# Performance work log

Hardware: AMD Instinct MI355X
Metric: run time of the kernel (lower is better)

Reference implementation:

```python
import jax, jax.numpy as jnp
import numpy as np

B = 512        # batch of parallel sequences
TM1 = 64       # T-1 recurrence steps
BELIEF = 2048  # GRU / deterministic belief size
STATE = 256    # stochastic state size
ACTION = 64
HIDDEN = 2048
EMB = 1024     # embedding_size['fusion']
MIN_STD = 0.1


def setup_inputs() -> dict:
    key = jax.random.key(0)
    ks = jax.random.split(key, 16)
    w = lambda k, shape: jax.random.normal(k, shape, dtype=jnp.float32) * 0.02
    return {
        "prev_state": jax.random.normal(ks[0], (B, STATE), dtype=jnp.float32),
        "actions": jax.random.normal(ks[1], (TM1, B, ACTION), dtype=jnp.float32),
        "prev_belief": jax.random.normal(ks[2], (B, BELIEF), dtype=jnp.float32),
        "obs_emb": jax.random.normal(ks[3], (TM1, B, EMB), dtype=jnp.float32),
        "nonterminals": jnp.ones((TM1, B, 1), dtype=jnp.float32),
        # fc_embed_state_action
        "W_embed": w(ks[4], (STATE + ACTION, BELIEF)),
        "b_embed": jnp.zeros((BELIEF,), jnp.float32),
        # GRUCell (input-to-hidden / hidden-to-hidden, gate order r,z,n as torch)
        "Wi": w(ks[5], (BELIEF, 3 * BELIEF)),
        "bi": jnp.zeros((3 * BELIEF,), jnp.float32),
        "Wh": w(ks[6], (BELIEF, 3 * BELIEF)),
        "bh": jnp.zeros((3 * BELIEF,), jnp.float32),
        # stochastic_state_model (prior): h -> hidden -> 2*state
        "W1": w(ks[7], (BELIEF, HIDDEN)),
        "b1": jnp.zeros((HIDDEN,), jnp.float32),
        "W2": w(ks[8], (HIDDEN, 2 * STATE)),
        "b2": jnp.zeros((2 * STATE,), jnp.float32),
        # obs_encoder (posterior): cat(h, obs_emb) -> hidden -> 2*state
        "W1p": w(ks[9], (BELIEF + EMB, HIDDEN)),
        "b1p": jnp.zeros((HIDDEN,), jnp.float32),
        "W2p": w(ks[10], (HIDDEN, 2 * STATE)),
        "b2p": jnp.zeros((2 * STATE,), jnp.float32),
        # reparameterized-sampling noise (rsample = loc + scale * eps)
        "eps_prior": jax.random.normal(ks[11], (TM1, B, STATE), dtype=jnp.float32),
        "eps_post": jax.random.normal(ks[12], (TM1, B, STATE), dtype=jnp.float32),
    }


def reference(prev_state, actions, prev_belief, obs_emb, nonterminals,
              W_embed, b_embed, Wi, bi, Wh, bh,
              W1, b1, W2, b2, W1p, b1p, W2p, b2p,
              eps_prior, eps_post):
    def step(carry, xs):
        belief, post_state = carry
        a, obs, nt, ep, eq = xs
        s = post_state * nt                                   # [B, S]
        hidden = jax.nn.relu(jnp.concatenate([s, a], axis=1) @ W_embed + b_embed)
        # torch.nn.GRUCell math (gate order r, z, n)
        gi = hidden @ Wi + bi
        gh = belief @ Wh + bh
        i_r, i_z, i_n = jnp.split(gi, 3, axis=1)
        h_r, h_z, h_n = jnp.split(gh, 3, axis=1)
        r = jax.nn.sigmoid(i_r + h_r)
        z = jax.nn.sigmoid(i_z + h_z)
        n = jnp.tanh(i_n + r * h_n)
        new_belief = (1.0 - z) * n + z * belief               # [B, H]
        # prior stochastic state model
        hp = jax.nn.relu(new_belief @ W1 + b1)
        loc_p, raw_p = jnp.split(hp @ W2 + b2, 2, axis=1)
        scale_p = jax.nn.softplus(raw_p) + MIN_STD
        prior_state = loc_p + scale_p * ep                    # rsample
        # posterior from obs embedding
        hq = jax.nn.relu(jnp.concatenate([new_belief, obs], axis=1) @ W1p + b1p)
        loc_q, raw_q = jnp.split(hq @ W2p + b2p, 2, axis=1)
        scale_q = jax.nn.softplus(raw_q) + MIN_STD
        post_new = loc_q + scale_q * eq                       # rsample
        ys = (new_belief, prior_state, loc_p, scale_p, post_new, loc_q, scale_q)
        return (new_belief, post_new), ys

    _, ys = jax.lax.scan(step, (prev_belief, prev_state),
                         (actions, obs_emb, nonterminals, eps_prior, eps_post))
    # (beliefs, prior_states, prior_means, prior_std_devs,
    #  posterior_states, posterior_means, posterior_std_devs), each [T-1, B, ...]
    return ys
```

## Files before the change

kernel.cpp:

```cpp
#include <hip/hip_runtime.h>
#include <hip/hip_bf16.h>
#include <cstdint>

typedef __hip_bfloat16 bf16;
typedef __attribute__((ext_vector_type(8))) short bf16x8v;
typedef __attribute__((ext_vector_type(4))) float f32x4;

#define TM1 64
#define BATCH 512
#define BELIEF 2048
#define STATE 256
#define ACTION 64
#define HIDDEN 2048
#define EMB 1024

#define OUT_BEL  ((size_t)0)
#define OUT_PST  ((size_t)67108864)
#define OUT_PMU  ((size_t)75497472)
#define OUT_PSD  ((size_t)83886080)
#define OUT_QST  ((size_t)92274688)
#define OUT_QMU  ((size_t)100663296)
#define OUT_QSD  ((size_t)109051904)

__device__ __forceinline__ void gload_lds16(const bf16* g, bf16* l) {
  __builtin_amdgcn_global_load_lds(
      (const __attribute__((address_space(1))) unsigned int*)g,
      (__attribute__((address_space(3))) unsigned int*)l, 16, 0, 0);
}

__device__ __forceinline__ unsigned short bfb(float f) {
  bf16 h = __float2bfloat16(f);
  return *reinterpret_cast<unsigned short*>(&h);
}

struct GDesc {
  const bf16* A; const bf16* B; const float* bias; void* C;
  int M, N, K, mode, nb;
};

template<int BM, int BN>
__global__ __launch_bounds__(256)
void gemm2(GDesc d0, GDesc d1)
{
  const int nwg = gridDim.x;
  const int orig = blockIdx.x;
  const int q8 = nwg >> 3, r8 = nwg & 7;
  const int xcd = orig & 7, oo = orig >> 3;
  int bid = (xcd < r8 ? xcd * (q8 + 1) : r8 * (q8 + 1) + (xcd - r8) * q8) + oo;

  GDesc d = d0;
  if (bid >= d.nb) { bid -= d.nb; d = d1; }

  const int nm = d.M / BM;
  const int mb = bid % nm;
  const int nbk = bid / nm;
  const int m0 = mb * BM, n0 = nbk * BN;

  __shared__ __align__(16) bf16 sA[2][BM * 64];
  __shared__ __align__(16) bf16 sB[2][BN * 64];

  const int tid = threadIdx.x;
  const int lane = tid & 63;
  const int wid = tid >> 6;
  const int wm = wid >> 1, wn = wid & 1;
  const int lr = lane & 15;
  const int ko = (lane >> 4) * 8;
  constexpr int WMt = BM / 2, WNt = BN / 2;
  constexpr int MR = WMt / 16, NR = WNt / 16;

  const bf16* Abase = d.A + (size_t)m0 * d.K;
  const bf16* Bbase = d.B + (size_t)n0 * d.K;
  const int K = d.K;

  auto stage = [&](int buf, int k0) {
    #pragma unroll
    for (int i = 0; i < BM / 32; ++i) {
      int c = i * 256 + tid;
      gload_lds16(Abase + (size_t)(c >> 3) * K + k0 + (c & 7) * 8, &sA[buf][c * 8]);
    }
    #pragma unroll
    for (int i = 0; i < BN / 32; ++i) {
      int c = i * 256 + tid;
      gload_lds16(Bbase + (size_t)(c >> 3) * K + k0 + (c & 7) * 8, &sB[buf][c * 8]);
    }
  };

  f32x4 acc[MR][NR] = {};

  stage(0, 0);
  __syncthreads();
  const int nk = K >> 6;
  for (int it = 0; it < nk; ++it) {
    const int cur = it & 1;
    if (it + 1 < nk) stage(cur ^ 1, (it + 1) << 6);
    #pragma unroll
    for (int kk = 0; kk < 2; ++kk) {
      bf16x8v af[MR], bfv[NR];
      #pragma unroll
      for (int m = 0; m < MR; ++m)
        af[m] = *(const bf16x8v*)&sA[cur][(wm * WMt + m * 16 + lr) * 64 + kk * 32 + ko];
      #pragma unroll
      for (int n = 0; n < NR; ++n)
        bfv[n] = *(const bf16x8v*)&sB[cur][(wn * WNt + n * 16 + lr) * 64 + kk * 32 + ko];
      #pragma unroll
      for (int m = 0; m < MR; ++m)
        #pragma unroll
        for (int n = 0; n < NR; ++n)
          acc[m][n] = __builtin_amdgcn_mfma_f32_16x16x32_bf16(af[m], bfv[n], acc[m][n], 0, 0, 0);
    }
    __syncthreads();
  }

  const int r0 = (lane >> 4) * 4;
  #pragma unroll
  for (int m = 0; m < MR; ++m) {
    #pragma unroll
    for (int n = 0; n < NR; ++n) {
      int gc = n0 + wn * WNt + n * 16 + lr;
      float bv = d.bias[gc];
      #pragma unroll
      for (int r = 0; r < 4; ++r) {
        int gr = m0 + wm * WMt + m * 16 + r0 + r;
        float v = acc[m][n][r] + bv;
        if (d.mode == 1)
          ((bf16*)d.C)[(size_t)gr * d.N + gc] = __float2bfloat16(v > 0.f ? v : 0.f);
        else
          ((float*)d.C)[(size_t)gr * d.N + gc] = v;
      }
    }
  }
}

__global__ __launch_bounds__(256)
void w2p_post(const bf16* __restrict__ hq, const bf16* __restrict__ W2pT,
              const float* __restrict__ b2p, const float* __restrict__ eps,
              float* __restrict__ o_mu, float* __restrict__ o_sd,
              float* __restrict__ o_st,
              const float* __restrict__ nt_next, const float* __restrict__ act_next,
              bf16* __restrict__ xcat, int make_xcat)
{
  constexpr int K = 2048, NK = K / 64;
  const int mb = blockIdx.x & 7, nl = blockIdx.x >> 3;
  const int m0 = mb * 64;

  __shared__ __align__(16) char smem[49152];
  bf16 (*sA)[64 * 64]  = (bf16(*)[64 * 64])smem;
  bf16 (*sB)[128 * 64] = (bf16(*)[128 * 64])(smem + 16384);
  float* tile = (float*)smem;

  const int tid = threadIdx.x;
  const int lane = tid & 63;
  const int wid = tid >> 6;
  const int wm = wid >> 1, wn = wid & 1;
  const int lr = lane & 15;
  const int ko = (lane >> 4) * 8;

  const bf16* Abase = hq + (size_t)m0 * K;

  auto stage = [&](int buf, int k0) {
    #pragma unroll
    for (int i = 0; i < 2; ++i) {
      int c = i * 256 + tid;
      gload_lds16(Abase + (size_t)(c >> 3) * K + k0 + (c & 7) * 8, &sA[buf][c * 8]);
    }
    #pragma unroll
    for (int i = 0; i < 4; ++i) {
      int c = i * 256 + tid;
      int row = c >> 3;
      int grow = (row < 64) ? (nl * 64 + row) : (192 + nl * 64 + row);
      gload_lds16(W2pT + (size_t)grow * K + k0 + (c & 7) * 8, &sB[buf][c * 8]);
    }
  };

  f32x4 acc[2][4] = {};
  stage(0, 0);
  __syncthreads();
  for (int it = 0; it < NK; ++it) {
    const int cur = it & 1;
    if (it + 1 < NK) stage(cur ^ 1, (it + 1) << 6);
    #pragma unroll
    for (int kk = 0; kk < 2; ++kk) {
      bf16x8v af[2], bfv[4];
      #pragma unroll
      for (int m = 0; m < 2; ++m)
        af[m] = *(const bf16x8v*)&sA[cur][(wm * 32 + m * 16 + lr) * 64 + kk * 32 + ko];
      #pragma unroll
      for (int n = 0; n < 4; ++n)
        bfv[n] = *(const bf16x8v*)&sB[cur][(wn * 64 + n * 16 + lr) * 64 + kk * 32 + ko];
      #pragma unroll
      for (int m = 0; m < 2; ++m)
        #pragma unroll
        for (int n = 0; n < 4; ++n)
          acc[m][n] = __builtin_amdgcn_mfma_f32_16x16x32_bf16(af[m], bfv[n], acc[m][n], 0, 0, 0);
    }
    __syncthreads();
  }

  const int r0 = (lane >> 4) * 4;
  #pragma unroll
  for (int m = 0; m < 2; ++m)
    #pragma unroll
    for (int n = 0; n < 4; ++n) {
      int tc = wn * 64 + n * 16 + lr;
      #pragma unroll
      for (int r = 0; r < 4; ++r)
        tile[(wm * 32 + m * 16 + r0 + r) * 128 + tc] = acc[m][n][r];
    }
  __syncthreads();

  for (int e = tid; e < 4096; e += 256) {
    int rr = e >> 6, cc = e & 63;
    int b = m0 + rr;
    int j = nl * 64 + cc;
    float loc = tile[rr * 128 + cc] + b2p[j];
    float raw = tile[rr * 128 + 64 + cc] + b2p[256 + j];
    float sp = (raw > 20.f) ? raw : log1pf(__expf(raw));
    float scale = sp + 0.1f;
    float st = loc + scale * eps[(size_t)b * 256 + j];
    o_mu[(size_t)b * 256 + j] = loc;
    o_sd[(size_t)b * 256 + j] = scale;
    o_st[(size_t)b * 256 + j] = st;
    if (make_xcat) {
      xcat[(size_t)b * 320 + j] = __float2bfloat16(st * nt_next[b]);
      if (nl == 0)
        xcat[(size_t)b * 320 + 256 + cc] = __float2bfloat16(act_next[(size_t)b * 64 + cc]);
    }
  }
}

__global__ void transpose_cvt(const float* __restrict__ src, bf16* __restrict__ dst,
                              int K, int N)
{
  __shared__ float t[32][33];
  int n0 = blockIdx.x * 32, k0 = blockIdx.y * 32;
  int tx = threadIdx.x, ty = threadIdx.y;
  #pragma unroll
  for (int i = 0; i < 32; i += 8)
    t[ty + i][tx] = src[(size_t)(k0 + ty + i) * N + n0 + tx];
  __syncthreads();
  #pragma unroll
  for (int i = 0; i < 32; i += 8)
    dst[(size_t)(n0 + ty + i) * K + k0 + tx] = __float2bfloat16(t[tx][ty + i]);
}

__global__ void init_belief(const float* __restrict__ prev_belief,
                            float* __restrict__ bf32, bf16* __restrict__ bb16)
{
  int i = blockIdx.x * 256 + threadIdx.x;
  float v = prev_belief[i];
  bf32[i] = v;
  bb16[i] = __float2bfloat16(v);
}

__global__ void xcat0_kernel(const float* __restrict__ prev_state,
                             const float* __restrict__ nt0,
                             const float* __restrict__ act0,
                             bf16* __restrict__ xcat)
{
  int idx = blockIdx.x * 256 + threadIdx.x;
  if (idx >= BATCH * 320) return;
  int b = idx / 320;
  int c = idx - b * 320;
  float v;
  if (c < STATE) v = prev_state[b * STATE + c] * nt0[b];
  else           v = act0[b * ACTION + (c - STATE)];
  xcat[idx] = __float2bfloat16(v);
}

__device__ __forceinline__ float sigmoidf_(float x) { return 1.f / (1.f + __expf(-x)); }

__device__ __forceinline__ float gru1(float ir, float hr, float iz, float hz,
                                      float in_, float hn, float bo)
{
  float r = sigmoidf_(ir + hr);
  float z = sigmoidf_(iz + hz);
  float n = tanhf(in_ + r * hn);
  return (1.f - z) * n + z * bo;
}

__global__ void gru_ew(const float* __restrict__ gi, const float* __restrict__ gh,
                       float* __restrict__ belief, float* __restrict__ out_bel,
                       bf16* __restrict__ belief_b16, bf16* __restrict__ hqcat,
                       const float* __restrict__ obs_t)
{
  int i = blockIdx.x * 256 + threadIdx.x;
  int b = i >> 9;
  int c = (i & 511) * 4;
  size_t gb = (size_t)b * 6144;
  float4 ir = *(const float4*)&gi[gb + c];
  float4 iz = *(const float4*)&gi[gb + 2048 + c];
  float4 in_ = *(const float4*)&gi[gb + 4096 + c];
  float4 hr = *(const float4*)&gh[gb + c];
  float4 hz = *(const float4*)&gh[gb + 2048 + c];
  float4 hn = *(const float4*)&gh[gb + 4096 + c];
  float4 bo = *(const float4*)&belief[(size_t)b * 2048 + c];
  float4 nb;
  nb.x = gru1(ir.x, hr.x, iz.x, hz.x, in_.x, hn.x, bo.x);
  nb.y = gru1(ir.y, hr.y, iz.y, hz.y, in_.y, hn.y, bo.y);
  nb.z = gru1(ir.z, hr.z, iz.z, hz.z, in_.z, hn.z, bo.z);
  nb.w = gru1(ir.w, hr.w, iz.w, hz.w, in_.w, hn.w, bo.w);
  *(float4*)&belief[(size_t)b * 2048 + c] = nb;
  *(float4*)&out_bel[(size_t)b * 2048 + c] = nb;
  ushort4 u; u.x = bfb(nb.x); u.y = bfb(nb.y); u.z = bfb(nb.z); u.w = bfb(nb.w);
  *(ushort4*)&belief_b16[(size_t)b * 2048 + c] = u;
  *(ushort4*)&hqcat[(size_t)b * 3072 + c] = u;
  if ((i & 511) < 256) {
    float4 ov = *(const float4*)&obs_t[(size_t)b * 1024 + c];
    ushort4 uo; uo.x = bfb(ov.x); uo.y = bfb(ov.y); uo.z = bfb(ov.z); uo.w = bfb(ov.w);
    *(ushort4*)&hqcat[(size_t)b * 3072 + 2048 + c] = uo;
  }
}

__global__ void cvt_f32_bf16(const float* __restrict__ src, bf16* __restrict__ dst)
{
  int i = blockIdx.x * 256 + threadIdx.x;
  float4 v = *(const float4*)&src[i * 4];
  ushort4 u; u.x = bfb(v.x); u.y = bfb(v.y); u.z = bfb(v.z); u.w = bfb(v.w);
  *(ushort4*)&dst[i * 4] = u;
}

__global__ void prior_ew(const float* __restrict__ yp, const float* __restrict__ eps,
                         float* __restrict__ o_mu, float* __restrict__ o_sd,
                         float* __restrict__ o_st)
{
  int idx = blockIdx.x * 256 + threadIdx.x;
  int r = idx >> 8;
  int j = idx & 255;
  float loc = yp[(size_t)r * 512 + j];
  float raw = yp[(size_t)r * 512 + 256 + j];
  float sp = (raw > 20.f) ? raw : log1pf(__expf(raw));
  float scale = sp + 0.1f;
  o_mu[idx] = loc;
  o_sd[idx] = scale;
  o_st[idx] = loc + scale * eps[idx];
}

extern "C" void kernel_launch(void* const* d_in, const int* in_sizes, int n_in,
                              void* d_out, int out_size, void* d_ws, size_t ws_size,
                              hipStream_t stream)
{
  (void)in_sizes; (void)n_in; (void)out_size; (void)ws_size;
  const float* prev_state = (const float*)d_in[0];
  const float* actions    = (const float*)d_in[1];
  const float* prev_belief= (const float*)d_in[2];
  const float* obs_emb    = (const float*)d_in[3];
  const float* nonterm    = (const float*)d_in[4];
  const float* W_embed    = (const float*)d_in[5];
  const float* b_embed    = (const float*)d_in[6];
  const float* Wi         = (const float*)d_in[7];
  const float* bi         = (const float*)d_in[8];
  const float* Wh         = (const float*)d_in[9];
  const float* bh         = (const float*)d_in[10];
  const float* W1         = (const float*)d_in[11];
  const float* b1         = (const float*)d_in[12];
  const float* W2         = (const float*)d_in[13];
  const float* b2         = (const float*)d_in[14];
  const float* W1p        = (const float*)d_in[15];
  const float* b1p        = (const float*)d_in[16];
  const float* W2p        = (const float*)d_in[17];
  const float* b2p        = (const float*)d_in[18];
  const float* eps_p      = (const float*)d_in[19];
  const float* eps_q      = (const float*)d_in[20];
  float* out = (float*)d_out;

  char* ws = (char*)d_ws;
  size_t off = 0;
  auto alloc = [&](size_t bytes) -> char* {
    char* p = ws + off;
    off = (off + bytes + 255) & ~(size_t)255;
    return p;
  };
  bf16* WembT = (bf16*)alloc((size_t)2048 * 320 * 2);
  bf16* WiT   = (bf16*)alloc((size_t)6144 * 2048 * 2);
  bf16* WhT   = (bf16*)alloc((size_t)6144 * 2048 * 2);
  bf16* W1T   = (bf16*)alloc((size_t)2048 * 2048 * 2);
  bf16* W2T   = (bf16*)alloc((size_t)512 * 2048 * 2);
  bf16* W1pT  = (bf16*)alloc((size_t)2048 * 3072 * 2);
  bf16* W2pT  = (bf16*)alloc((size_t)512 * 2048 * 2);
  float* belief_f32 = (float*)alloc((size_t)BATCH * BELIEF * 4);
  bf16*  belief_b16 = (bf16*)alloc((size_t)BATCH * BELIEF * 2);
  bf16*  xcat       = (bf16*)alloc((size_t)BATCH * 320 * 2);
  bf16*  hidden     = (bf16*)alloc((size_t)BATCH * BELIEF * 2);
  float* gi         = (float*)alloc((size_t)BATCH * 3 * BELIEF * 4);
  float* gh         = (float*)alloc((size_t)BATCH * 3 * BELIEF * 4);
  bf16*  hqcat      = (bf16*)alloc((size_t)BATCH * 3072 * 2);
  bf16*  hq         = (bf16*)alloc((size_t)BATCH * HIDDEN * 2);
  bf16*  belA       = (bf16*)alloc((size_t)4096 * BELIEF * 2);
  bf16*  hp         = (bf16*)alloc((size_t)4096 * HIDDEN * 2);
  float* yp         = (float*)alloc((size_t)4096 * 512 * 4);

  auto mk = [](const bf16* A, const bf16* B, const float* bias, void* C,
               int M, int N, int K, int mode, int BM, int BN) {
    GDesc g; g.A = A; g.B = B; g.bias = bias; g.C = C;
    g.M = M; g.N = N; g.K = K; g.mode = mode;
    g.nb = (M / BM) * (N / BN);
    return g;
  };
  GDesc dz{}; dz.nb = 0;

  dim3 tb(32, 8);
  transpose_cvt<<<dim3(2048/32, 320/32),  tb, 0, stream>>>(W_embed, WembT, 320, 2048);
  transpose_cvt<<<dim3(6144/32, 2048/32), tb, 0, stream>>>(Wi, WiT, 2048, 6144);
  transpose_cvt<<<dim3(6144/32, 2048/32), tb, 0, stream>>>(Wh, WhT, 2048, 6144);
  transpose_cvt<<<dim3(2048/32, 2048/32), tb, 0, stream>>>(W1, W1T, 2048, 2048);
  transpose_cvt<<<dim3(512/32, 2048/32),  tb, 0, stream>>>(W2, W2T, 2048, 512);
  transpose_cvt<<<dim3(2048/32, 3072/32), tb, 0, stream>>>(W1p, W1pT, 3072, 2048);
  transpose_cvt<<<dim3(512/32, 2048/32),  tb, 0, stream>>>(W2p, W2pT, 2048, 512);

  init_belief<<<(BATCH * BELIEF) / 256, 256, 0, stream>>>(prev_belief, belief_f32, belief_b16);
  xcat0_kernel<<<(BATCH * 320 + 255) / 256, 256, 0, stream>>>(prev_state, nonterm, actions, xcat);

  {
    GDesc e = mk(xcat, WembT, b_embed, hidden, 512, 2048, 320, 1, 64, 64);
    gemm2<64,64><<<e.nb, 256, 0, stream>>>(e, dz);
  }

  for (int t = 0; t < TM1; ++t) {
    GDesc a0 = mk(hidden, WiT, bi, gi, 512, 6144, 2048, 0, 128, 96);
    GDesc a1 = mk(belief_b16, WhT, bh, gh, 512, 6144, 2048, 0, 128, 96);
    gemm2<128,96><<<a0.nb + a1.nb, 256, 0, stream>>>(a0, a1);

    gru_ew<<<1024, 256, 0, stream>>>(
        gi, gh, belief_f32,
        out + OUT_BEL + (size_t)t * BATCH * BELIEF,
        belief_b16, hqcat, obs_emb + (size_t)t * BATCH * EMB);

    GDesc b0 = mk(hqcat, W1pT, b1p, hq, 512, 2048, 3072, 1, 64, 64);
    gemm2<64,64><<<b0.nb, 256, 0, stream>>>(b0, dz);

    int tn = (t < TM1 - 1) ? t + 1 : t;
    w2p_post<<<32, 256, 0, stream>>>(
        hq, W2pT, b2p,
        eps_q + (size_t)t * BATCH * STATE,
        out + OUT_QMU + (size_t)t * BATCH * STATE,
        out + OUT_QSD + (size_t)t * BATCH * STATE,
        out + OUT_QST + (size_t)t * BATCH * STATE,
        nonterm + (size_t)tn * BATCH,
        actions + (size_t)tn * BATCH * ACTION,
        xcat, (t < TM1 - 1) ? 1 : 0);

    if (t < TM1 - 1) {
      GDesc e = mk(xcat, WembT, b_embed, hidden, 512, 2048, 320, 1, 64, 64);
      gemm2<64,64><<<e.nb, 256, 0, stream>>>(e, dz);
    }
  }

  for (int c = 0; c < 8; ++c) {
    const float* belsrc = out + OUT_BEL + (size_t)c * 4096 * BELIEF;
    cvt_f32_bf16<<<(4096 * BELIEF / 4) / 256, 256, 0, stream>>>(belsrc, belA);
    GDesc p1 = mk(belA, W1T, b1, hp, 4096, 2048, 2048, 1, 128, 128);
    gemm2<128,128><<<p1.nb, 256, 0, stream>>>(p1, dz);
    GDesc p2 = mk(hp, W2T, b2, yp, 4096, 512, 2048, 0, 64, 64);
    gemm2<64,64><<<p2.nb, 256, 0, stream>>>(p2, dz);
    prior_ew<<<4096, 256, 0, stream>>>(
        yp, eps_p + (size_t)c * 4096 * STATE,
        out + OUT_PMU + (size_t)c * 4096 * STATE,
        out + OUT_PSD + (size_t)c * 4096 * STATE,
        out + OUT_PST + (size_t)c * 4096 * STATE);
  }
}
```

Before: 10.02 ms.

## Fuse all stages into one persistent kernel with grid-wide atomic barriers

```diff
diff --git a/kernel.cpp b/kernel.cpp
--- a/kernel.cpp
+++ b/kernel.cpp
@@ -6,13 +6,9 @@
 typedef __attribute__((ext_vector_type(8))) short bf16x8v;
 typedef __attribute__((ext_vector_type(4))) float f32x4;
 
+#define NB 256
 #define TM1 64
 #define BATCH 512
-#define BELIEF 2048
-#define STATE 256
-#define ACTION 64
-#define HIDDEN 2048
-#define EMB 1024
 
 #define OUT_BEL  ((size_t)0)
 #define OUT_PST  ((size_t)67108864)
@@ -33,33 +29,29 @@
   return *reinterpret_cast<unsigned short*>(&h);
 }
 
-struct GDesc {
-  const bf16* A; const bf16* B; const float* bias; void* C;
-  int M, N, K, mode, nb;
-};
+__device__ __forceinline__ void gbar(unsigned* cnt, unsigned target) {
+  __syncthreads();
+  if (threadIdx.x == 0) {
+    __threadfence();
+    __hip_atomic_fetch_add(cnt, 1u, __ATOMIC_RELAXED, __HIP_MEMORY_SCOPE_AGENT);
+    while (__hip_atomic_load(cnt, __ATOMIC_RELAXED, __HIP_MEMORY_SCOPE_AGENT) < target)
+      __builtin_amdgcn_s_sleep(2);
+    __threadfence();
+  }
+  __syncthreads();
+}
 
 template<int BM, int BN>
-__global__ __launch_bounds__(256)
-void gemm2(GDesc d0, GDesc d1)
-{
-  const int nwg = gridDim.x;
-  const int orig = blockIdx.x;
-  const int q8 = nwg >> 3, r8 = nwg & 7;
-  const int xcd = orig & 7, oo = orig >> 3;
-  int bid = (xcd < r8 ? xcd * (q8 + 1) : r8 * (q8 + 1) + (xcd - r8) * q8) + oo;
-
-  GDesc d = d0;
-  if (bid >= d.nb) { bid -= d.nb; d = d1; }
-
-  const int nm = d.M / BM;
-  const int mb = bid % nm;
-  const int nbk = bid / nm;
-  const int m0 = mb * BM, n0 = nbk * BN;
-
-  __shared__ __align__(16) bf16 sA[2][BM * 64];
-  __shared__ __align__(16) bf16 sB[2][BN * 64];
-
-  const int tid = threadIdx.x;
+__device__ void gemm_tile(const bf16* __restrict__ A, const bf16* __restrict__ B,
+                          const float* __restrict__ bias, void* __restrict__ C,
+                          int N, int K, int nm, int mode, int job, int tid,
+                          char* pool)
+{
+  bf16 (*sA)[BM * 64] = (bf16(*)[BM * 64])pool;
+  bf16 (*sB)[BN * 64] = (bf16(*)[BN * 64])(pool + 2 * BM * 64 * 2);
+
+  const int m0 = (job % nm) * BM;
+  const int n0 = (job / nm) * BN;
   const int lane = tid & 63;
   const int wid = tid >> 6;
   const int wm = wid >> 1, wn = wid & 1;
@@ -68,9 +60,8 @@
   constexpr int WMt = BM / 2, WNt = BN / 2;
   constexpr int MR = WMt / 16, NR = WNt / 16;
 
-  const bf16* Abase = d.A + (size_t)m0 * d.K;
-  const bf16* Bbase = d.B + (size_t)n0 * d.K;
-  const int K = d.K;
+  const bf16* Abase = A + (size_t)m0 * K;
+  const bf16* Bbase = B + (size_t)n0 * K;
 
   auto stage = [&](int buf, int k0) {
     #pragma unroll
@@ -86,7 +77,7 @@
   };
 
   f32x4 acc[MR][NR] = {};
-
+  __syncthreads();
   stage(0, 0);
   __syncthreads();
   const int nk = K >> 6;
@@ -117,38 +108,37 @@
     #pragma unroll
     for (int n = 0; n < NR; ++n) {
       int gc = n0 + wn * WNt + n * 16 + lr;
-      float bv = d.bias[gc];
+      float bv = bias[gc];
       #pragma unroll
       for (int r = 0; r < 4; ++r) {
         int gr = m0 + wm * WMt + m * 16 + r0 + r;
         float v = acc[m][n][r] + bv;
-        if (d.mode == 1)
-          ((bf16*)d.C)[(size_t)gr * d.N + gc] = __float2bfloat16(v > 0.f ? v : 0.f);
+        if (mode == 1)
+          ((bf16*)C)[(size_t)gr * N + gc] = __float2bfloat16(v > 0.f ? v : 0.f);
         else
-          ((float*)d.C)[(size_t)gr * d.N + gc] = v;
+          ((float*)C)[(size_t)gr * N + gc] = v;
       }
     }
   }
 }
 
-__global__ __launch_bounds__(256)
-void w2p_post(const bf16* __restrict__ hq, const bf16* __restrict__ W2pT,
-              const float* __restrict__ b2p, const float* __restrict__ eps,
-              float* __restrict__ o_mu, float* __restrict__ o_sd,
-              float* __restrict__ o_st,
-              const float* __restrict__ nt_next, const float* __restrict__ act_next,
-              bf16* __restrict__ xcat, int make_xcat)
+__device__ void w2p_tile(const bf16* __restrict__ hq, const bf16* __restrict__ W2pT,
+                         const float* __restrict__ b2p, const float* __restrict__ eps,
+                         float* __restrict__ o_mu, float* __restrict__ o_sd,
+                         float* __restrict__ o_st,
+                         const float* __restrict__ nt_next,
+                         const float* __restrict__ act_next,
+                         bf16* __restrict__ xcat, int make_xcat,
+                         int blk, int tid, char* pool)
 {
   constexpr int K = 2048, NK = K / 64;
-  const int mb = blockIdx.x & 7, nl = blockIdx.x >> 3;
+  const int mb = blk & 7, nl = blk >> 3;
   const int m0 = mb * 64;
 
-  __shared__ __align__(16) char smem[49152];
-  bf16 (*sA)[64 * 64]  = (bf16(*)[64 * 64])smem;
-  bf16 (*sB)[128 * 64] = (bf16(*)[128 * 64])(smem + 16384);
-  float* tile = (float*)smem;
-
-  const int tid = threadIdx.x;
+  bf16 (*sA)[64 * 64]  = (bf16(*)[64 * 64])pool;
+  bf16 (*sB)[128 * 64] = (bf16(*)[128 * 64])(pool + 16384);
+  float* tile = (float*)pool;
+
   const int lane = tid & 63;
   const int wid = tid >> 6;
   const int wm = wid >> 1, wn = wid & 1;
@@ -173,6 +163,7 @@
   };
 
   f32x4 acc[2][4] = {};
+  __syncthreads();
   stage(0, 0);
   __syncthreads();
   for (int it = 0; it < NK; ++it) {
@@ -228,43 +219,23 @@
   }
 }
 
-__global__ void transpose_cvt(const float* __restrict__ src, bf16* __restrict__ dst,
-                              int K, int N)
-{
-  __shared__ float t[32][33];
-  int n0 = blockIdx.x * 32, k0 = blockIdx.y * 32;
-  int tx = threadIdx.x, ty = threadIdx.y;
-  #pragma unroll
-  for (int i = 0; i < 32; i += 8)
-    t[ty + i][tx] = src[(size_t)(k0 + ty + i) * N + n0 + tx];
-  __syncthreads();
-  #pragma unroll
-  for (int i = 0; i < 32; i += 8)
-    dst[(size_t)(n0 + ty + i) * K + k0 + tx] = __float2bfloat16(t[tx][ty + i]);
-}
-
-__global__ void init_belief(const float* __restrict__ prev_belief,
-                            float* __restrict__ bf32, bf16* __restrict__ bb16)
-{
-  int i = blockIdx.x * 256 + threadIdx.x;
-  float v = prev_belief[i];
-  bf32[i] = v;
-  bb16[i] = __float2bfloat16(v);
-}
-
-__global__ void xcat0_kernel(const float* __restrict__ prev_state,
-                             const float* __restrict__ nt0,
-                             const float* __restrict__ act0,
-                             bf16* __restrict__ xcat)
-{
-  int idx = blockIdx.x * 256 + threadIdx.x;
-  if (idx >= BATCH * 320) return;
-  int b = idx / 320;
-  int c = idx - b * 320;
-  float v;
-  if (c < STATE) v = prev_state[b * STATE + c] * nt0[b];
-  else           v = act0[b * ACTION + (c - STATE)];
-  xcat[idx] = __float2bfloat16(v);
+__device__ void transpose_phase(const float* __restrict__ src, bf16* __restrict__ dst,
+                                int K, int N, int bid, int tid, float* t )
+{
+  const int ntile = (K / 32) * (N / 32);
+  const int tx = tid & 31, ty = tid >> 5;
+  for (int it = bid; it < ntile; it += NB) {
+    int kt = it % (K / 32), nt = it / (K / 32);
+    int k0 = kt * 32, n0 = nt * 32;
+    __syncthreads();
+    #pragma unroll
+    for (int i = 0; i < 32; i += 8)
+      t[(ty + i) * 33 + tx] = src[(size_t)(k0 + ty + i) * N + n0 + tx];
+    __syncthreads();
+    #pragma unroll
+    for (int i = 0; i < 32; i += 8)
+      dst[(size_t)(n0 + ty + i) * K + k0 + tx] = __float2bfloat16(t[tx * 33 + ty + i]);
+  }
 }
 
 __device__ __forceinline__ float sigmoidf_(float x) { return 1.f / (1.f + __expf(-x)); }
@@ -278,61 +249,140 @@
   return (1.f - z) * n + z * bo;
 }
 
-__global__ void gru_ew(const float* __restrict__ gi, const float* __restrict__ gh,
-                       float* __restrict__ belief, float* __restrict__ out_bel,
-                       bf16* __restrict__ belief_b16, bf16* __restrict__ hqcat,
-                       const float* __restrict__ obs_t)
-{
-  int i = blockIdx.x * 256 + threadIdx.x;
-  int b = i >> 9;
-  int c = (i & 511) * 4;
-  size_t gb = (size_t)b * 6144;
-  float4 ir = *(const float4*)&gi[gb + c];
-  float4 iz = *(const float4*)&gi[gb + 2048 + c];
-  float4 in_ = *(const float4*)&gi[gb + 4096 + c];
-  float4 hr = *(const float4*)&gh[gb + c];
-  float4 hz = *(const float4*)&gh[gb + 2048 + c];
-  float4 hn = *(const float4*)&gh[gb + 4096 + c];
-  float4 bo = *(const float4*)&belief[(size_t)b * 2048 + c];
-  float4 nb;
-  nb.x = gru1(ir.x, hr.x, iz.x, hz.x, in_.x, hn.x, bo.x);
-  nb.y = gru1(ir.y, hr.y, iz.y, hz.y, in_.y, hn.y, bo.y);
-  nb.z = gru1(ir.z, hr.z, iz.z, hz.z, in_.z, hn.z, bo.z);
-  nb.w = gru1(ir.w, hr.w, iz.w, hz.w, in_.w, hn.w, bo.w);
-  *(float4*)&belief[(size_t)b * 2048 + c] = nb;
-  *(float4*)&out_bel[(size_t)b * 2048 + c] = nb;
-  ushort4 u; u.x = bfb(nb.x); u.y = bfb(nb.y); u.z = bfb(nb.z); u.w = bfb(nb.w);
-  *(ushort4*)&belief_b16[(size_t)b * 2048 + c] = u;
-  *(ushort4*)&hqcat[(size_t)b * 3072 + c] = u;
-  if ((i & 511) < 256) {
-    float4 ov = *(const float4*)&obs_t[(size_t)b * 1024 + c];
-    ushort4 uo; uo.x = bfb(ov.x); uo.y = bfb(ov.y); uo.z = bfb(ov.z); uo.w = bfb(ov.w);
-    *(ushort4*)&hqcat[(size_t)b * 3072 + 2048 + c] = uo;
-  }
-}
-
-__global__ void cvt_f32_bf16(const float* __restrict__ src, bf16* __restrict__ dst)
-{
-  int i = blockIdx.x * 256 + threadIdx.x;
-  float4 v = *(const float4*)&src[i * 4];
-  ushort4 u; u.x = bfb(v.x); u.y = bfb(v.y); u.z = bfb(v.z); u.w = bfb(v.w);
-  *(ushort4*)&dst[i * 4] = u;
-}
-
-__global__ void prior_ew(const float* __restrict__ yp, const float* __restrict__ eps,
-                         float* __restrict__ o_mu, float* __restrict__ o_sd,
-                         float* __restrict__ o_st)
-{
-  int idx = blockIdx.x * 256 + threadIdx.x;
-  int r = idx >> 8;
-  int j = idx & 255;
-  float loc = yp[(size_t)r * 512 + j];
-  float raw = yp[(size_t)r * 512 + 256 + j];
-  float sp = (raw > 20.f) ? raw : log1pf(__expf(raw));
-  float scale = sp + 0.1f;
-  o_mu[idx] = loc;
-  o_sd[idx] = scale;
-  o_st[idx] = loc + scale * eps[idx];
+struct Args {
+  const float *prev_state, *actions, *prev_belief, *obs_emb, *nonterm;
+  const float *W_embed, *b_embed, *Wi, *bi, *Wh, *bh;
+  const float *W1, *b1, *W2, *b2, *W1p, *b1p, *W2p, *b2p;
+  const float *eps_p, *eps_q;
+  bf16 *WembT, *WiT, *WhT, *W1T, *W2T, *W1pT, *W2pT;
+  float* belief_f32; bf16 *belief_b16, *xcat, *hidden;
+  float *gi, *gh; bf16 *hqcat, *hq, *belA, *hp; float* yp;
+  float* out;
+  unsigned* cnt;
+};
+
+__global__ __launch_bounds__(256) void mega(Args a)
+{
+  extern __shared__ char pool[];
+  const int bid = blockIdx.x;
+  const int tid = threadIdx.x;
+  const int sj = ((bid & 7) << 5) | (bid >> 3);
+  unsigned tgt = 0;
+
+  transpose_phase(a.W_embed, a.WembT, 320, 2048, bid, tid, (float*)pool);
+  transpose_phase(a.Wi,  a.WiT,  2048, 6144, bid, tid, (float*)pool);
+  transpose_phase(a.Wh,  a.WhT,  2048, 6144, bid, tid, (float*)pool);
+  transpose_phase(a.W1,  a.W1T,  2048, 2048, bid, tid, (float*)pool);
+  transpose_phase(a.W2,  a.W2T,  2048, 512,  bid, tid, (float*)pool);
+  transpose_phase(a.W1p, a.W1pT, 3072, 2048, bid, tid, (float*)pool);
+  transpose_phase(a.W2p, a.W2pT, 2048, 512,  bid, tid, (float*)pool);
+  for (int i = bid * 256 + tid; i < 512 * 2048; i += NB * 256) {
+    float v = a.prev_belief[i];
+    a.belief_f32[i] = v;
+    a.belief_b16[i] = __float2bfloat16(v);
+  }
+  for (int i = bid * 256 + tid; i < 512 * 320; i += NB * 256) {
+    int b = i / 320, c = i - b * 320;
+    float v = (c < 256) ? a.prev_state[b * 256 + c] * a.nonterm[b]
+                        : a.actions[b * 64 + (c - 256)];
+    a.xcat[i] = __float2bfloat16(v);
+  }
+  gbar(a.cnt, tgt += NB);
+
+  gemm_tile<64, 64>(a.xcat, a.WembT, a.b_embed, a.hidden, 2048, 320, 8, 1, sj, tid, pool);
+  gbar(a.cnt, tgt += NB);
+
+  for (int t = 0; t < TM1; ++t) {
+    gemm_tile<128, 96>(a.hidden, a.WiT, a.bi, a.gi, 6144, 2048, 4, 0, sj, tid, pool);
+    gemm_tile<128, 96>(a.belief_b16, a.WhT, a.bh, a.gh, 6144, 2048, 4, 0, sj, tid, pool);
+    gbar(a.cnt, tgt += NB);
+
+    {
+      const float* obs_t = a.obs_emb + (size_t)t * 512 * 1024;
+      float* out_bel = a.out + OUT_BEL + (size_t)t * 512 * 2048;
+      for (int i = bid * 256 + tid; i < 512 * 2048 / 4; i += NB * 256) {
+        int b = i >> 9;
+        int c = (i & 511) * 4;
+        size_t gb = (size_t)b * 6144;
+        float4 ir = *(const float4*)&a.gi[gb + c];
+        float4 iz = *(const float4*)&a.gi[gb + 2048 + c];
+        float4 in_ = *(const float4*)&a.gi[gb + 4096 + c];
+        float4 hr = *(const float4*)&a.gh[gb + c];
+        float4 hz = *(const float4*)&a.gh[gb + 2048 + c];
+        float4 hn = *(const float4*)&a.gh[gb + 4096 + c];
+        float4 bo = *(const float4*)&a.belief_f32[(size_t)b * 2048 + c];
+        float4 nb;
+        nb.x = gru1(ir.x, hr.x, iz.x, hz.x, in_.x, hn.x, bo.x);
+        nb.y = gru1(ir.y, hr.y, iz.y, hz.y, in_.y, hn.y, bo.y);
+        nb.z = gru1(ir.z, hr.z, iz.z, hz.z, in_.z, hn.z, bo.z);
+        nb.w = gru1(ir.w, hr.w, iz.w, hz.w, in_.w, hn.w, bo.w);
+        *(float4*)&a.belief_f32[(size_t)b * 2048 + c] = nb;
+        *(float4*)&out_bel[(size_t)b * 2048 + c] = nb;
+        ushort4 u; u.x = bfb(nb.x); u.y = bfb(nb.y); u.z = bfb(nb.z); u.w = bfb(nb.w);
+        *(ushort4*)&a.belief_b16[(size_t)b * 2048 + c] = u;
+        *(ushort4*)&a.hqcat[(size_t)b * 3072 + c] = u;
+        if ((i & 511) < 256) {
+          float4 ov = *(const float4*)&obs_t[(size_t)b * 1024 + c];
+          ushort4 uo; uo.x = bfb(ov.x); uo.y = bfb(ov.y); uo.z = bfb(ov.z); uo.w = bfb(ov.w);
+          *(ushort4*)&a.hqcat[(size_t)b * 3072 + 2048 + c] = uo;
+        }
+      }
+    }
+    gbar(a.cnt, tgt += NB);
+
+    gemm_tile<64, 64>(a.hqcat, a.W1pT, a.b1p, a.hq, 2048, 3072, 8, 1, sj, tid, pool);
+    gbar(a.cnt, tgt += NB);
+
+    {
+      int tn = (t < TM1 - 1) ? t + 1 : t;
+      if (bid < 32)
+        w2p_tile(a.hq, a.W2pT, a.b2p,
+                 a.eps_q + (size_t)t * 512 * 256,
+                 a.out + OUT_QMU + (size_t)t * 512 * 256,
+                 a.out + OUT_QSD + (size_t)t * 512 * 256,
+                 a.out + OUT_QST + (size_t)t * 512 * 256,
+                 a.nonterm + (size_t)tn * 512,
+                 a.actions + (size_t)tn * 512 * 64,
+                 a.xcat, (t < TM1 - 1) ? 1 : 0, bid, tid, pool);
+    }
+    gbar(a.cnt, tgt += NB);
+
+    if (t < TM1 - 1) {
+      gemm_tile<64, 64>(a.xcat, a.WembT, a.b_embed, a.hidden, 2048, 320, 8, 1, sj, tid, pool);
+      gbar(a.cnt, tgt += NB);
+    }
+  }
+
+  for (int c = 0; c < 8; ++c) {
+    const float* bsrc = a.out + OUT_BEL + (size_t)c * 4096 * 2048;
+    for (int i = bid * 256 + tid; i < 4096 * 2048 / 4; i += NB * 256) {
+      float4 v = *(const float4*)&bsrc[i * 4];
+      ushort4 u; u.x = bfb(v.x); u.y = bfb(v.y); u.z = bfb(v.z); u.w = bfb(v.w);
+      *(ushort4*)&a.belA[i * 4] = u;
+    }
+    gbar(a.cnt, tgt += NB);
+
+    gemm_tile<128, 128>(a.belA, a.W1T, a.b1, a.hp, 2048, 2048, 32, 1, sj, tid, pool);
+    gemm_tile<128, 128>(a.belA, a.W1T, a.b1, a.hp, 2048, 2048, 32, 1, sj + 256, tid, pool);
+    gbar(a.cnt, tgt += NB);
+
+    gemm_tile<64, 64>(a.hp, a.W2T, a.b2, a.yp, 512, 2048, 64, 0, sj, tid, pool);
+    gemm_tile<64, 64>(a.hp, a.W2T, a.b2, a.yp, 512, 2048, 64, 0, sj + 256, tid, pool);
+    gbar(a.cnt, tgt += NB);
+
+    for (int i = bid * 256 + tid; i < 4096 * 256; i += NB * 256) {
+      int r = i >> 8, j = i & 255;
+      float loc = a.yp[(size_t)r * 512 + j];
+      float raw = a.yp[(size_t)r * 512 + 256 + j];
+      float sp = (raw > 20.f) ? raw : log1pf(__expf(raw));
+      float scale = sp + 0.1f;
+      size_t o = (size_t)c * 4096 * 256 + i;
+      a.out[OUT_PMU + o] = loc;
+      a.out[OUT_PSD + o] = scale;
+      a.out[OUT_PST + o] = loc + scale * a.eps_p[o];
+    }
+    gbar(a.cnt, tgt += NB);
+  }
 }
 
 extern "C" void kernel_launch(void* const* d_in, const int* in_sizes, int n_in,
@@ -340,28 +390,29 @@
                               hipStream_t stream)
 {
   (void)in_sizes; (void)n_in; (void)out_size; (void)ws_size;
-  const float* prev_state = (const float*)d_in[0];
-  const float* actions    = (const float*)d_in[1];
-  const float* prev_belief= (const float*)d_in[2];
-  const float* obs_emb    = (const float*)d_in[3];
-  const float* nonterm    = (const float*)d_in[4];
-  const float* W_embed    = (const float*)d_in[5];
-  const float* b_embed    = (const float*)d_in[6];
-  const float* Wi         = (const float*)d_in[7];
-  const float* bi         = (const float*)d_in[8];
-  const float* Wh         = (const float*)d_in[9];
-  const float* bh         = (const float*)d_in[10];
-  const float* W1         = (const float*)d_in[11];
-  const float* b1         = (const float*)d_in[12];
-  const float* W2         = (const float*)d_in[13];
-  const float* b2         = (const float*)d_in[14];
-  const float* W1p        = (const float*)d_in[15];
-  const float* b1p        = (const float*)d_in[16];
-  const float* W2p        = (const float*)d_in[17];
-  const float* b2p        = (const float*)d_in[18];
-  const float* eps_p      = (const float*)d_in[19];
-  const float* eps_q      = (const float*)d_in[20];
-  float* out = (float*)d_out;
+  Args a;
+  a.prev_state = (const float*)d_in[0];
+  a.actions    = (const float*)d_in[1];
+  a.prev_belief= (const float*)d_in[2];
+  a.obs_emb    = (const float*)d_in[3];
+  a.nonterm    = (const float*)d_in[4];
+  a.W_embed    = (const float*)d_in[5];
+  a.b_embed    = (const float*)d_in[6];
+  a.Wi         = (const float*)d_in[7];
+  a.bi         = (const float*)d_in[8];
+  a.Wh         = (const float*)d_in[9];
+  a.bh         = (const float*)d_in[10];
+  a.W1         = (const float*)d_in[11];
+  a.b1         = (const float*)d_in[12];
+  a.W2         = (const float*)d_in[13];
+  a.b2         = (const float*)d_in[14];
+  a.W1p        = (const float*)d_in[15];
+  a.b1p        = (const float*)d_in[16];
+  a.W2p        = (const float*)d_in[17];
+  a.b2p        = (const float*)d_in[18];
+  a.eps_p      = (const float*)d_in[19];
+  a.eps_q      = (const float*)d_in[20];
+  a.out        = (float*)d_out;
 
   char* ws = (char*)d_ws;
   size_t off = 0;
@@ -370,92 +421,26 @@
     off = (off + bytes + 255) & ~(size_t)255;
     return p;
   };
-  bf16* WembT = (bf16*)alloc((size_t)2048 * 320 * 2);
-  bf16* WiT   = (bf16*)alloc((size_t)6144 * 2048 * 2);
-  bf16* WhT   = (bf16*)alloc((size_t)6144 * 2048 * 2);
-  bf16* W1T   = (bf16*)alloc((size_t)2048 * 2048 * 2);
-  bf16* W2T   = (bf16*)alloc((size_t)512 * 2048 * 2);
-  bf16* W1pT  = (bf16*)alloc((size_t)2048 * 3072 * 2);
-  bf16* W2pT  = (bf16*)alloc((size_t)512 * 2048 * 2);
-  float* belief_f32 = (float*)alloc((size_t)BATCH * BELIEF * 4);
-  bf16*  belief_b16 = (bf16*)alloc((size_t)BATCH * BELIEF * 2);
-  bf16*  xcat       = (bf16*)alloc((size_t)BATCH * 320 * 2);
-  bf16*  hidden     = (bf16*)alloc((size_t)BATCH * BELIEF * 2);
-  float* gi         = (float*)alloc((size_t)BATCH * 3 * BELIEF * 4);
-  float* gh         = (float*)alloc((size_t)BATCH * 3 * BELIEF * 4);
-  bf16*  hqcat      = (bf16*)alloc((size_t)BATCH * 3072 * 2);
-  bf16*  hq         = (bf16*)alloc((size_t)BATCH * HIDDEN * 2);
-  bf16*  belA       = (bf16*)alloc((size_t)4096 * BELIEF * 2);
-  bf16*  hp         = (bf16*)alloc((size_t)4096 * HIDDEN * 2);
-  float* yp         = (float*)alloc((size_t)4096 * 512 * 4);
-
-  auto mk = [](const bf16* A, const bf16* B, const float* bias, void* C,
-               int M, int N, int K, int mode, int BM, int BN) {
-    GDesc g; g.A = A; g.B = B; g.bias = bias; g.C = C;
-    g.M = M; g.N = N; g.K = K; g.mode = mode;
-    g.nb = (M / BM) * (N / BN);
-    return g;
-  };
-  GDesc dz{}; dz.nb = 0;
-
-  dim3 tb(32, 8);
-  transpose_cvt<<<dim3(2048/32, 320/32),  tb, 0, stream>>>(W_embed, WembT, 320, 2048);
-  transpose_cvt<<<dim3(6144/32, 2048/32), tb, 0, stream>>>(Wi, WiT, 2048, 6144);
-  transpose_cvt<<<dim3(6144/32, 2048/32), tb, 0, stream>>>(Wh, WhT, 2048, 6144);
-  transpose_cvt<<<dim3(2048/32, 2048/32), tb, 0, stream>>>(W1, W1T, 2048, 2048);
-  transpose_cvt<<<dim3(512/32, 2048/32),  tb, 0, stream>>>(W2, W2T, 2048, 512);
-  transpose_cvt<<<dim3(2048/32, 3072/32), tb, 0, stream>>>(W1p, W1pT, 3072, 2048);
-  transpose_cvt<<<dim3(512/32, 2048/32),  tb, 0, stream>>>(W2p, W2pT, 2048, 512);
-
-  init_belief<<<(BATCH * BELIEF) / 256, 256, 0, stream>>>(prev_belief, belief_f32, belief_b16);
-  xcat0_kernel<<<(BATCH * 320 + 255) / 256, 256, 0, stream>>>(prev_state, nonterm, actions, xcat);
-
-  {
-    GDesc e = mk(xcat, WembT, b_embed, hidden, 512, 2048, 320, 1, 64, 64);
-    gemm2<64,64><<<e.nb, 256, 0, stream>>>(e, dz);
-  }
-
-  for (int t = 0; t < TM1; ++t) {
-    GDesc a0 = mk(hidden, WiT, bi, gi, 512, 6144, 2048, 0, 128, 96);
-    GDesc a1 = mk(belief_b16, WhT, bh, gh, 512, 6144, 2048, 0, 128, 96);
-    gemm2<128,96><<<a0.nb + a1.nb, 256, 0, stream>>>(a0, a1);
-
-    gru_ew<<<1024, 256, 0, stream>>>(
-        gi, gh, belief_f32,
-        out + OUT_BEL + (size_t)t * BATCH * BELIEF,
-        belief_b16, hqcat, obs_emb + (size_t)t * BATCH * EMB);
-
-    GDesc b0 = mk(hqcat, W1pT, b1p, hq, 512, 2048, 3072, 1, 64, 64);
-    gemm2<64,64><<<b0.nb, 256, 0, stream>>>(b0, dz);
-
-    int tn = (t < TM1 - 1) ? t + 1 : t;
-    w2p_post<<<32, 256, 0, stream>>>(
-        hq, W2pT, b2p,
-        eps_q + (size_t)t * BATCH * STATE,
-        out + OUT_QMU + (size_t)t * BATCH * STATE,
-        out + OUT_QSD + (size_t)t * BATCH * STATE,
-        out + OUT_QST + (size_t)t * BATCH * STATE,
-        nonterm + (size_t)tn * BATCH,
-        actions + (size_t)tn * BATCH * ACTION,
-        xcat, (t < TM1 - 1) ? 1 : 0);
-
-    if (t < TM1 - 1) {
-      GDesc e = mk(xcat, WembT, b_embed, hidden, 512, 2048, 320, 1, 64, 64);
-      gemm2<64,64><<<e.nb, 256, 0, stream>>>(e, dz);
-    }
-  }
-
-  for (int c = 0; c < 8; ++c) {
-    const float* belsrc = out + OUT_BEL + (size_t)c * 4096 * BELIEF;
-    cvt_f32_bf16<<<(4096 * BELIEF / 4) / 256, 256, 0, stream>>>(belsrc, belA);
-    GDesc p1 = mk(belA, W1T, b1, hp, 4096, 2048, 2048, 1, 128, 128);
-    gemm2<128,128><<<p1.nb, 256, 0, stream>>>(p1, dz);
-    GDesc p2 = mk(hp, W2T, b2, yp, 4096, 512, 2048, 0, 64, 64);
-    gemm2<64,64><<<p2.nb, 256, 0, stream>>>(p2, dz);
-    prior_ew<<<4096, 256, 0, stream>>>(
-        yp, eps_p + (size_t)c * 4096 * STATE,
-        out + OUT_PMU + (size_t)c * 4096 * STATE,
-        out + OUT_PSD + (size_t)c * 4096 * STATE,
-        out + OUT_PST + (size_t)c * 4096 * STATE);
-  }
-}
+  a.cnt        = (unsigned*)alloc(256);
+  a.WembT      = (bf16*)alloc((size_t)2048 * 320 * 2);
+  a.WiT        = (bf16*)alloc((size_t)6144 * 2048 * 2);
+  a.WhT        = (bf16*)alloc((size_t)6144 * 2048 * 2);
+  a.W1T        = (bf16*)alloc((size_t)2048 * 2048 * 2);
+  a.W2T        = (bf16*)alloc((size_t)512 * 2048 * 2);
+  a.W1pT       = (bf16*)alloc((size_t)2048 * 3072 * 2);
+  a.W2pT       = (bf16*)alloc((size_t)512 * 2048 * 2);
+  a.belief_f32 = (float*)alloc((size_t)512 * 2048 * 4);
+  a.belief_b16 = (bf16*)alloc((size_t)512 * 2048 * 2);
+  a.xcat       = (bf16*)alloc((size_t)512 * 320 * 2);
+  a.hidden     = (bf16*)alloc((size_t)512 * 2048 * 2);
+  a.gi         = (float*)alloc((size_t)512 * 6144 * 4);
+  a.gh         = (float*)alloc((size_t)512 * 6144 * 4);
+  a.hqcat      = (bf16*)alloc((size_t)512 * 3072 * 2);
+  a.hq         = (bf16*)alloc((size_t)512 * 2048 * 2);
+  a.belA       = (bf16*)alloc((size_t)4096 * 2048 * 2);
+  a.hp         = (bf16*)alloc((size_t)4096 * 2048 * 2);
+  a.yp         = (float*)alloc((size_t)4096 * 512 * 4);
+
+  hipMemsetAsync(a.cnt, 0, 256, stream);
+  mega<<<NB, 256, 65536, stream>>>(a);
+}
```

Result: slower. 17.01 ms (+69.7%).
